# Optimization experiments

Measured on AMD Instinct MI355X. Metric: run time of the kernel, lower is better.

Reference implementation:

```python
import jax, jax.numpy as jnp
import numpy as np
import math

HEAD_DIM = 64           # d_model // n_heads // 2
N_HEADS = 8
LAMBDA_INIT = 0.8 - 0.6 * math.exp(-0.3 * 6)  # depth=6
EPS = 1e-5


def setup_inputs() -> dict:
    key = jax.random.key(0)
    ks = jax.random.split(key, 8)
    B, T, S = 2, 2048, 2048
    return {
        "queries": jax.random.normal(ks[0], (B, 2 * N_HEADS, T, HEAD_DIM), jnp.float32),
        "keys": jax.random.normal(ks[1], (B, 2 * N_HEADS, S, HEAD_DIM), jnp.float32),
        "values": jax.random.normal(ks[2], (B, N_HEADS, S, 2 * HEAD_DIM), jnp.float32),
        "lambda_q1": 0.02 * jax.random.normal(ks[3], (HEAD_DIM,), jnp.float32),
        "lambda_k1": 0.02 * jax.random.normal(ks[4], (HEAD_DIM,), jnp.float32),
        "lambda_q2": 0.02 * jax.random.normal(ks[5], (HEAD_DIM,), jnp.float32),
        "lambda_k2": 0.02 * jax.random.normal(ks[6], (HEAD_DIM,), jnp.float32),
        "subln_weight": jnp.ones((2 * HEAD_DIM,), jnp.float32),
        "tgt_len": 2048,
        "src_len": 2048,
        "attn_mask": jnp.zeros((1,), jnp.bool_),
    }


def reference(queries, keys, values, lambda_q1, lambda_k1, lambda_q2, lambda_k2,
              subln_weight, tgt_len, src_len, attn_mask):
    B = queries.shape[0]
    scaling = HEAD_DIM ** -0.5
    q = queries * scaling
    # [B, 2H, T, S]
    attn_w = jnp.einsum('bhtd,bhsd->bhts', q, keys)
    attn_w = jax.nn.softmax(attn_w.astype(jnp.float32), axis=-1).astype(queries.dtype)
    lam1 = jnp.exp(jnp.sum(lambda_q1 * lambda_k1))
    lam2 = jnp.exp(jnp.sum(lambda_q2 * lambda_k2))
    lam_full = lam1 - lam2 + LAMBDA_INIT
    attn_w = attn_w.reshape(B, N_HEADS, 2, tgt_len, src_len)
    attn_w = attn_w[:, :, 0] - lam_full * attn_w[:, :, 1]   # [B, H, T, S]
    attn = jnp.einsum('bhts,bhse->bhte', attn_w, values)    # [B, H, T, 2*HEAD_DIM]
    # RMSNorm over last dim
    normed = attn * jax.lax.rsqrt(jnp.mean(jnp.square(attn.astype(jnp.float32)), axis=-1, keepdims=True) + EPS).astype(attn.dtype)
    normed = normed * subln_weight
    out = normed * (1.0 - LAMBDA_INIT)
    out = out.transpose(0, 2, 1, 3).reshape(B, tgt_len, N_HEADS * 2 * HEAD_DIM)
    return out
```

## Files before the change

### kernel.cpp

```cpp
#include <hip/hip_runtime.h>
#include <math.h>


#define NT    2048
#define D     64
#define DV    128
#define TQ    64
#define TS    32
#define NROUND (NT / (2 * TS))

#define LAMBDA_INIT 0.70082066706704814f
#define OUT_SCALE   0.29917933293295186f

typedef __attribute__((ext_vector_type(8)))  short    short8;
typedef __attribute__((ext_vector_type(4)))  short    short4v;
typedef __attribute__((ext_vector_type(8)))  _Float16 half8;
typedef __attribute__((ext_vector_type(4)))  float    f32x4;
typedef unsigned short u16;
typedef unsigned int   u32;

#define MFMAH(a, b, c)  __builtin_amdgcn_mfma_f32_16x16x32_f16(a, b, c, 0, 0, 0)
#define MFMA16(a, b, c) __builtin_amdgcn_mfma_f32_16x16x32_bf16(a, b, c, 0, 0, 0)

union Hu { half8 v; _Float16 e[8]; u16 s[8]; short8 sv; };

__device__ __forceinline__ u16 f2h(float x) {
    Hu u; u.e[0] = (_Float16)x; return u.s[0];
}

__global__ __launch_bounds__(256) void prep_k(
    const float* __restrict__ Kg,
    const float* __restrict__ lq1, const float* __restrict__ lk1,
    const float* __restrict__ lq2, const float* __restrict__ lk2,
    u16* __restrict__ Kf, float* __restrict__ lamw)
{
    const int bid = blockIdx.x;
    const int t   = threadIdx.x;
    if (bid == 2048) {
        if (t == 0) {
            float t1 = 0.f, t2 = 0.f;
            for (int i = 0; i < D; ++i) {
                t1 = fmaf(lq1[i], lk1[i], t1);
                t2 = fmaf(lq2[i], lk2[i], t2);
            }
            lamw[0] = __expf(t1) - __expf(t2) + LAMBDA_INIT;
        }
        return;
    }
    const int idx = (bid * 256 + t) * 8;
    const float4 a = *(const float4*)(Kg + idx);
    const float4 b = *(const float4*)(Kg + idx + 4);
    Hu H;
    H.e[0] = (_Float16)a.x; H.e[1] = (_Float16)a.y;
    H.e[2] = (_Float16)a.z; H.e[3] = (_Float16)a.w;
    H.e[4] = (_Float16)b.x; H.e[5] = (_Float16)b.y;
    H.e[6] = (_Float16)b.z; H.e[7] = (_Float16)b.w;
    *(short8*)(Kf + idx) = H.sv;
}

__global__ __launch_bounds__(256) void prep_v(const float* __restrict__ Vg,
                                              u16* __restrict__ Vf)
{
    __shared__ u16 th[64 * 136];
    const int i  = blockIdx.x;
    const int t  = threadIdx.x;
    const int bh = i >> 5;
    const int eb = (i >> 4) & 1;
    const int sb = i & 15;
    const size_t vbase = (size_t)bh * NT * DV + (size_t)sb * 128 * DV + eb * 64;
    {
        const int r0 = t >> 4;
        const int c4 = (t & 15) * 4;
        #pragma unroll
        for (int rr = 0; rr < 8; ++rr) {
            const int row = r0 + rr * 16;
            const float4 x = *(const float4*)(Vg + vbase + (size_t)row * DV + c4);
            th[(c4 + 0) * 136 + row] = f2h(x.x);
            th[(c4 + 1) * 136 + row] = f2h(x.y);
            th[(c4 + 2) * 136 + row] = f2h(x.z);
            th[(c4 + 3) * 136 + row] = f2h(x.w);
        }
    }
    __syncthreads();
    const int e  = t >> 2;
    const int g  = t & 3;
    const size_t orow = ((size_t)bh * DV + eb * 64 + e) * NT + sb * 128;
    #pragma unroll
    for (int c = 0; c < 4; ++c) {
        Hu o;
        #pragma unroll
        for (int j = 0; j < 8; ++j)
            o.s[j] = th[e * 136 + g * 32 + 4 * c + (j & 3) + 16 * (j >> 2)];
        *(short8*)(Vf + orow + g * 32 + c * 8) = o.sv;
    }
}

struct SmemF {
    union {
        short8 c[2048];
        struct {
            float epi[2][32][132];
            float lbuf[2][2][2][32];
        } e;
    };
};

__global__ __launch_bounds__(512, 4) void diffattn_mfma10(
    const float* __restrict__ Qg,
    const u16* __restrict__ Kf, const u16* __restrict__ Vf,
    const float* __restrict__ lamw,
    const float* __restrict__ Wg, float* __restrict__ Outg)
{
    __shared__ SmemF sm;

    const int tid    = threadIdx.x;
    const int wv     = tid >> 6;
    const int lane   = tid & 63;
    const int quad   = lane >> 4;
    const int lc     = lane & 15;
    const int stripe = wv & 1;
    const int hh     = (wv >> 1) & 1;
    const int ks     = wv >> 2;
    const int wig    = wv & 3;
    const int qt     = blockIdx.x;
    const int bh     = blockIdx.y;
    const int b      = bh >> 3, h = bh & 7;

    const int head2b = b * 16 + 2 * h;
    const int bh8    = b * 8 + h;
    const float lam  = lamw[0];

    half8 qf[2][2];
    {
        const size_t qhead = (size_t)(head2b + hh) * NT * D;
        #pragma unroll
        for (int nq = 0; nq < 2; ++nq) {
            const int row = qt * TQ + stripe * 32 + nq * 16 + lc;
            #pragma unroll
            for (int k0 = 0; k0 < 2; ++k0) {
                const int d0 = k0 * 32 + quad * 8;
                const float4 x = *(const float4*)(Qg + qhead + (size_t)row * D + d0);
                const float4 y = *(const float4*)(Qg + qhead + (size_t)row * D + d0 + 4);
                Hu q;
                q.e[0] = (_Float16)(x.x * 0.125f); q.e[1] = (_Float16)(x.y * 0.125f);
                q.e[2] = (_Float16)(x.z * 0.125f); q.e[3] = (_Float16)(x.w * 0.125f);
                q.e[4] = (_Float16)(y.x * 0.125f); q.e[5] = (_Float16)(y.y * 0.125f);
                q.e[6] = (_Float16)(y.z * 0.125f); q.e[7] = (_Float16)(y.w * 0.125f);
                qf[nq][k0] = q.v;
            }
        }
    }

    f32x4 O_[2][8];
    #pragma unroll
    for (int nq = 0; nq < 2; ++nq)
        #pragma unroll
        for (int nt = 0; nt < 8; ++nt) O_[nq][nt] = (f32x4){0.f, 0.f, 0.f, 0.f};
    float lac[2] = {0.f, 0.f};

    u32 gK[2], gV[2];
    int kDst[2], vDst[2];
    #pragma unroll
    for (int j = 0; j < 2; ++j) {
        const int ck  = wig * 128 + lane * 2 + j;
        const int hhs = ck >> 8;
        const int n   = (ck >> 3) & 31;
        const int db  = ck & 7;
        gK[j]   = (u32)(((head2b + hhs) * NT + n) * D + db * 8);
        kDst[j] = ks * 512 + hhs * 256 + n * 8 + (db ^ (n & 7));
        const int cv = wig * 128 + lane * 2 + j;
        const int e  = cv >> 2;
        const int u  = cv & 3;
        gV[j]   = (u32)((bh8 * DV + e) * NT + u * 8);
        vDst[j] = 1024 + ks * 512 + e * 4 + (u ^ ((e >> 1) & 3));
    }

    short8 pk[2], pv[2];
    #pragma unroll
    for (int j = 0; j < 2; ++j) {
        pk[j] = *(const short8*)(Kf + gK[j] + (u32)ks * (TS * D));
        pv[j] = *(const short8*)(Vf + gV[j] + (u32)ks * TS);
    }

    u32 kOff[2][2];
    #pragma unroll
    for (int k0 = 0; k0 < 2; ++k0)
        #pragma unroll
        for (int mt = 0; mt < 2; ++mt)
            kOff[k0][mt] = (u32)((ks * 512 + hh * 256 + (mt * 16 + lc) * 8 +
                                  ((4 * k0 + quad) ^ (lc & 7))) * 8);
    u32 vOff[8];
    {
        const int swzv = quad ^ ((lc >> 1) & 3);
        #pragma unroll
        for (int nt = 0; nt < 8; ++nt)
            vOff[nt] = (u32)((1024 + ks * 512 + (nt * 16 + lc) * 4 + swzv) * 8);
    }

    const u16* ldsu = (const u16*)&sm.c[0];

    for (int r = 0; r < NROUND; ++r) {
        sm.c[kDst[0]] = pk[0];
        sm.c[kDst[1]] = pk[1];
        sm.c[vDst[0]] = pv[0];
        sm.c[vDst[1]] = pv[1];
        __syncthreads();

        if (r < NROUND - 1) {
            const u32 tn = (u32)(2 * r + 2 + ks);
            #pragma unroll
            for (int j = 0; j < 2; ++j) {
                pk[j] = *(const short8*)(Kf + gK[j] + tn * (TS * D));
                pv[j] = *(const short8*)(Vf + gV[j] + tn * TS);
            }
        }

        f32x4 sf[2][2];
        #pragma unroll
        for (int mt = 0; mt < 2; ++mt)
            #pragma unroll
            for (int nq = 0; nq < 2; ++nq) sf[mt][nq] = (f32x4){0.f, 0.f, 0.f, 0.f};
        #pragma unroll
        for (int k0 = 0; k0 < 2; ++k0) {
            #pragma unroll
            for (int mt = 0; mt < 2; ++mt) {
                const half8 kfr = *(const half8*)(ldsu + kOff[k0][mt]);
                #pragma unroll
                for (int nq = 0; nq < 2; ++nq)
                    sf[mt][nq] = MFMAH(kfr, qf[nq][k0], sf[mt][nq]);
            }
        }

        half8 a8[2];
        #pragma unroll
        for (int nq = 0; nq < 2; ++nq) {
            Hu a;
            #pragma unroll
            for (int mt = 0; mt < 2; ++mt)
                #pragma unroll
                for (int i = 0; i < 4; ++i) {
                    const float p = __expf(sf[mt][nq][i]);
                    lac[nq] += p;
                    a.e[mt * 4 + i] = (_Float16)p;
                }
            a8[nq] = a.v;
        }

        #pragma unroll
        for (int nt = 0; nt < 8; ++nt) {
            const half8 vfr = *(const half8*)(ldsu + vOff[nt]);
            #pragma unroll
            for (int nq = 0; nq < 2; ++nq)
                O_[nq][nt] = MFMAH(a8[nq], vfr, O_[nq][nt]);
        }

        __syncthreads();
    }

    {
        float s0 = lac[0], s1 = lac[1];
        s0 += __shfl_xor(s0, 16); s0 += __shfl_xor(s0, 32);
        s1 += __shfl_xor(s1, 16); s1 += __shfl_xor(s1, 32);
        if (quad == 0) {
            sm.e.lbuf[hh][ks][stripe][lc]      = s0;
            sm.e.lbuf[hh][ks][stripe][16 + lc] = s1;
        }
    }
    __syncthreads();
    float coef[2][4];
    #pragma unroll
    for (int nq = 0; nq < 2; ++nq)
        #pragma unroll
        for (int i = 0; i < 4; ++i) {
            const int row = nq * 16 + quad * 4 + i;
            const float lt = sm.e.lbuf[hh][0][stripe][row] +
                             sm.e.lbuf[hh][1][stripe][row];
            coef[nq][i] = (hh == 0) ? (1.f / lt) : (-lam / lt);
        }
    __syncthreads();
    const int pid = hh * 2 + ks;
    #pragma unroll
    for (int p = 0; p < 4; ++p) {
        if (pid == p) {
            #pragma unroll
            for (int nq = 0; nq < 2; ++nq)
                #pragma unroll
                for (int i = 0; i < 4; ++i) {
                    const int row = nq * 16 + quad * 4 + i;
                    #pragma unroll
                    for (int nt = 0; nt < 8; ++nt) {
                        const int col = nt * 16 + lc;
                        const float v = O_[nq][nt][i] * coef[nq][i];
                        if (p == 0) sm.e.epi[stripe][row][col] = v;
                        else        sm.e.epi[stripe][row][col] += v;
                    }
                }
        }
        __syncthreads();
    }
    {
        const int r0 = wv * 8 + (lane >> 3);
        const int st = r0 >> 5, ri = r0 & 31;
        const int e0 = (lane & 7) * 16;
        float x[16];
        float ssq = 0.f;
        #pragma unroll
        for (int m = 0; m < 16; m += 4) {
            const float4 t4 = *(const float4*)&sm.e.epi[st][ri][e0 + m];
            x[m] = t4.x; x[m + 1] = t4.y; x[m + 2] = t4.z; x[m + 3] = t4.w;
            ssq += t4.x * t4.x + t4.y * t4.y + t4.z * t4.z + t4.w * t4.w;
        }
        ssq += __shfl_xor(ssq, 1);
        ssq += __shfl_xor(ssq, 2);
        ssq += __shfl_xor(ssq, 4);
        const float rsq = rsqrtf(ssq * (1.f / 128.f) + 1e-5f) * OUT_SCALE;
        const int rowg = qt * TQ + r0;
        const size_t base =
            ((size_t)b * NT + rowg) * (size_t)(8 * DV) + (size_t)h * DV;
        #pragma unroll
        for (int m = 0; m < 16; m += 4) {
            const float4 w4 = *(const float4*)(Wg + e0 + m);
            float4 o4;
            o4.x = x[m] * rsq * w4.x;
            o4.y = x[m + 1] * rsq * w4.y;
            o4.z = x[m + 2] * rsq * w4.z;
            o4.w = x[m + 3] * rsq * w4.w;
            *(float4*)(Outg + base + e0 + m) = o4;
        }
    }
}

__device__ __forceinline__ unsigned short f2bf(float x) {
    unsigned u = __float_as_uint(x);
    return (unsigned short)((u + 0x7fffu + ((u >> 16) & 1u)) >> 16);
}
__device__ __forceinline__ float bf2f(unsigned short h) {
    return __uint_as_float(((unsigned)h) << 16);
}

struct SmemB {
    union {
        struct {
            short8 kh[2][264];
            short8 kl[2][264];
            short8 vh[516];
            short8 vl[516];
            unsigned short ph[2][2560];
            unsigned short pl[2][2560];
        } L;
        float epi[2][32][132];
    };
};

__global__ __launch_bounds__(256, 2) void diffattn_fb(
    const float* __restrict__ Qg, const float* __restrict__ Kg,
    const float* __restrict__ Vg,
    const float* __restrict__ lq1, const float* __restrict__ lk1,
    const float* __restrict__ lq2, const float* __restrict__ lk2,
    const float* __restrict__ Wg, float* __restrict__ Outg)
{
    __shared__ SmemB sm;
    const int tid = threadIdx.x;
    const int wv = tid >> 6, lane = tid & 63;
    const int quad = lane >> 4, lc = lane & 15;
    const int stripe = wv & 1, hh = wv >> 1;
    const int qt = blockIdx.x, bh = blockIdx.y;
    const int b = bh >> 3, h = bh & 7;
    const size_t koff0 = ((size_t)(b * 16 + 2 * h)) * NT * D;
    const size_t voff  = ((size_t)(b * 8 + h)) * NT * DV;
    float t1 = 0.f, t2 = 0.f;
    for (int i = 0; i < D; ++i) {
        t1 = fmaf(lq1[i], lk1[i], t1);
        t2 = fmaf(lq2[i], lk2[i], t2);
    }
    const float lam = __expf(t1) - __expf(t2) + LAMBDA_INIT;
    short8 qfh[2][2], qfl[2][2];
    {
        const size_t qhead = ((size_t)(b * 16 + 2 * h + hh)) * NT * D;
        #pragma unroll
        for (int mt = 0; mt < 2; ++mt)
            #pragma unroll
            for (int k0 = 0; k0 < 2; ++k0) {
                const int row = qt * TQ + stripe * 32 + mt * 16 + lc;
                const int d0  = k0 * 32 + quad * 8;
                const float4 x = *(const float4*)(Qg + qhead + (size_t)row * D + d0);
                const float4 y = *(const float4*)(Qg + qhead + (size_t)row * D + d0 + 4);
                float f[8] = {x.x, x.y, x.z, x.w, y.x, y.y, y.z, y.w};
                #pragma unroll
                for (int j = 0; j < 8; ++j) {
                    const float v = f[j] * 0.125f;
                    const unsigned short hi = f2bf(v);
                    qfh[mt][k0][j] = (short)hi;
                    qfl[mt][k0][j] = (short)f2bf(v - bf2f(hi));
                }
            }
    }
    f32x4 O_[2][8];
    #pragma unroll
    for (int mt = 0; mt < 2; ++mt)
        #pragma unroll
        for (int nt = 0; nt < 8; ++nt) O_[mt][nt] = (f32x4){0.f, 0.f, 0.f, 0.f};
    float m_[2][4], l_[2][4], a_[2][4];
    #pragma unroll
    for (int mt = 0; mt < 2; ++mt)
        #pragma unroll
        for (int i = 0; i < 4; ++i) { m_[mt][i] = -1e30f; l_[mt][i] = 0.f; }
    const int s_hh = tid >> 7;
    const int s_n  = (tid >> 2) & 31;
    const int s_d0 = (tid & 3) * 16;
    const int s_e0 = tid & 31;
    const int s_s0 = ((tid >> 5) & 7) * 4;
    const int s_sb = s_s0 >> 3;
    const int s_hs = (s_s0 & 4) ? 1 : 0;
    for (int kt = 0; kt < NT / TS; ++kt) {
        const int kb = kt * TS;
        __syncthreads();
        {
            const float* kp = Kg + koff0 + (size_t)s_hh * NT * D +
                              (size_t)(kb + s_n) * D + s_d0;
            const float4 x0 = ((const float4*)kp)[0];
            const float4 x1 = ((const float4*)kp)[1];
            const float4 x2 = ((const float4*)kp)[2];
            const float4 x3 = ((const float4*)kp)[3];
            float f[16] = {x0.x, x0.y, x0.z, x0.w, x1.x, x1.y, x1.z, x1.w,
                           x2.x, x2.y, x2.z, x2.w, x3.x, x3.y, x3.z, x3.w};
            short8 c0h, c0l, c1h, c1l;
            #pragma unroll
            for (int j = 0; j < 8; ++j) {
                unsigned short hi = f2bf(f[j]);
                c0h[j] = (short)hi; c0l[j] = (short)f2bf(f[j] - bf2f(hi));
                hi = f2bf(f[8 + j]);
                c1h[j] = (short)hi; c1l[j] = (short)f2bf(f[8 + j] - bf2f(hi));
            }
            const int db0 = s_d0 >> 3;
            sm.L.kh[s_hh][db0 * 33 + s_n]       = c0h;
            sm.L.kl[s_hh][db0 * 33 + s_n]       = c0l;
            sm.L.kh[s_hh][(db0 + 1) * 33 + s_n] = c1h;
            sm.L.kl[s_hh][(db0 + 1) * 33 + s_n] = c1l;
        }
        {
            #pragma unroll
            for (int j = 0; j < 4; ++j) {
                const int e = s_e0 + 32 * j;
                float f[4];
                #pragma unroll
                for (int i = 0; i < 4; ++i)
                    f[i] = Vg[voff + (size_t)(kb + s_s0 + i) * DV + e];
                short4v hi4, lo4;
                #pragma unroll
                for (int i = 0; i < 4; ++i) {
                    const unsigned short hi = f2bf(f[i]);
                    hi4[i] = (short)hi;
                    lo4[i] = (short)f2bf(f[i] - bf2f(hi));
                }
                ((short4v*)&sm.L.vh[s_sb * 129 + e])[s_hs] = hi4;
                ((short4v*)&sm.L.vl[s_sb * 129 + e])[s_hs] = lo4;
            }
        }
        __syncthreads();
        f32x4 s_f[2][2];
        #pragma unroll
        for (int mt = 0; mt < 2; ++mt)
            #pragma unroll
            for (int nt = 0; nt < 2; ++nt) s_f[mt][nt] = (f32x4){0.f, 0.f, 0.f, 0.f};
        #pragma unroll
        for (int k0 = 0; k0 < 2; ++k0)
            #pragma unroll
            for (int nt = 0; nt < 2; ++nt) {
                const short8 kh = sm.L.kh[hh][(4 * k0 + quad) * 33 + nt * 16 + lc];
                const short8 kl = sm.L.kl[hh][(4 * k0 + quad) * 33 + nt * 16 + lc];
                #pragma unroll
                for (int mt = 0; mt < 2; ++mt) {
                    s_f[mt][nt] = MFMA16(qfh[mt][k0], kh, s_f[mt][nt]);
                    s_f[mt][nt] = MFMA16(qfl[mt][k0], kh, s_f[mt][nt]);
                    s_f[mt][nt] = MFMA16(qfh[mt][k0], kl, s_f[mt][nt]);
                }
            }
        #pragma unroll
        for (int mt = 0; mt < 2; ++mt)
            #pragma unroll
            for (int i = 0; i < 4; ++i) {
                const float v0 = s_f[mt][0][i], v1 = s_f[mt][1][i];
                float mx = fmaxf(v0, v1);
                mx = fmaxf(mx, __shfl_xor(mx, 1));
                mx = fmaxf(mx, __shfl_xor(mx, 2));
                mx = fmaxf(mx, __shfl_xor(mx, 4));
                mx = fmaxf(mx, __shfl_xor(mx, 8));
                const float mn = fmaxf(m_[mt][i], mx);
                const float al = __expf(m_[mt][i] - mn);
                const float p0 = __expf(v0 - mn);
                const float p1 = __expf(v1 - mn);
                float rs = p0 + p1;
                rs += __shfl_xor(rs, 1);
                rs += __shfl_xor(rs, 2);
                rs += __shfl_xor(rs, 4);
                rs += __shfl_xor(rs, 8);
                l_[mt][i] = l_[mt][i] * al + rs;
                m_[mt][i] = mn;
                a_[mt][i] = al;
                const int r = stripe * 32 + mt * 16 + quad * 4 + i;
                const unsigned short h0 = f2bf(p0);
                sm.L.ph[hh][r * 40 + lc]      = h0;
                sm.L.pl[hh][r * 40 + lc]      = f2bf(p0 - bf2f(h0));
                const unsigned short h1 = f2bf(p1);
                sm.L.ph[hh][r * 40 + 16 + lc] = h1;
                sm.L.pl[hh][r * 40 + 16 + lc] = f2bf(p1 - bf2f(h1));
            }
        __syncthreads();
        #pragma unroll
        for (int mt = 0; mt < 2; ++mt)
            #pragma unroll
            for (int nt = 0; nt < 8; ++nt)
                #pragma unroll
                for (int i = 0; i < 4; ++i) O_[mt][nt][i] *= a_[mt][i];
        short8 pah[2], pal[2];
        #pragma unroll
        for (int mt = 0; mt < 2; ++mt) {
            const int r = stripe * 32 + mt * 16 + lc;
            pah[mt] = *(const short8*)&sm.L.ph[hh][r * 40 + quad * 8];
            pal[mt] = *(const short8*)&sm.L.pl[hh][r * 40 + quad * 8];
        }
        #pragma unroll
        for (int nt = 0; nt < 8; ++nt) {
            const short8 vh = sm.L.vh[quad * 129 + nt * 16 + lc];
            const short8 vl = sm.L.vl[quad * 129 + nt * 16 + lc];
            #pragma unroll
            for (int mt = 0; mt < 2; ++mt) {
                O_[mt][nt] = MFMA16(pah[mt], vh, O_[mt][nt]);
                O_[mt][nt] = MFMA16(pal[mt], vh, O_[mt][nt]);
                O_[mt][nt] = MFMA16(pah[mt], vl, O_[mt][nt]);
            }
        }
    }
    __syncthreads();
    if (hh == 1) {
        #pragma unroll
        for (int mt = 0; mt < 2; ++mt)
            #pragma unroll
            for (int i = 0; i < 4; ++i) {
                const float inv = lam / l_[mt][i];
                const int r = mt * 16 + quad * 4 + i;
                #pragma unroll
                for (int nt = 0; nt < 8; ++nt)
                    sm.epi[stripe][r][nt * 16 + lc] = O_[mt][nt][i] * inv;
            }
    }
    __syncthreads();
    if (hh == 0) {
        float wvv[8];
        #pragma unroll
        for (int nt = 0; nt < 8; ++nt) wvv[nt] = Wg[nt * 16 + lc];
        #pragma unroll
        for (int mt = 0; mt < 2; ++mt)
            #pragma unroll
            for (int i = 0; i < 4; ++i) {
                const float inv1 = 1.f / l_[mt][i];
                const int r = mt * 16 + quad * 4 + i;
                float od[8];
                float ss = 0.f;
                #pragma unroll
                for (int nt = 0; nt < 8; ++nt) {
                    od[nt] = O_[mt][nt][i] * inv1 - sm.epi[stripe][r][nt * 16 + lc];
                    ss = fmaf(od[nt], od[nt], ss);
                }
                ss += __shfl_xor(ss, 1);
                ss += __shfl_xor(ss, 2);
                ss += __shfl_xor(ss, 4);
                ss += __shfl_xor(ss, 8);
                const float rsq = rsqrtf(ss * (1.f / 128.f) + 1e-5f) * OUT_SCALE;
                const int rowg = qt * TQ + stripe * 32 + r;
                const size_t base =
                    ((size_t)b * NT + rowg) * (size_t)(8 * DV) + (size_t)h * DV;
                #pragma unroll
                for (int nt = 0; nt < 8; ++nt)
                    Outg[base + nt * 16 + lc] = od[nt] * rsq * wvv[nt];
            }
    }
}

extern "C" void kernel_launch(void* const* d_in, const int* in_sizes, int n_in,
                              void* d_out, int out_size, void* d_ws, size_t ws_size,
                              hipStream_t stream) {
    const float* Q   = (const float*)d_in[0];
    const float* K   = (const float*)d_in[1];
    const float* V   = (const float*)d_in[2];
    const float* lq1 = (const float*)d_in[3];
    const float* lk1 = (const float*)d_in[4];
    const float* lq2 = (const float*)d_in[5];
    const float* lk2 = (const float*)d_in[6];
    const float* W   = (const float*)d_in[7];
    float* Out = (float*)d_out;
    const size_t NEED = 2ull * 4194304ull * sizeof(u16) + 16;
    if (ws_size >= NEED) {
        u16*   Kf   = (u16*)d_ws;
        u16*   Vf   = Kf + 4194304;
        float* lamw = (float*)(Vf + 4194304);
        prep_k<<<2049, 256, 0, stream>>>(K, lq1, lk1, lq2, lk2, Kf, lamw);
        prep_v<<<512, 256, 0, stream>>>(V, Vf);
        diffattn_mfma10<<<dim3(NT / TQ, 16), 512, 0, stream>>>(
            Q, Kf, Vf, lamw, W, Out);
    } else {
        diffattn_fb<<<dim3(NT / TQ, 16), 256, 0, stream>>>(
            Q, K, V, lq1, lk1, lq2, lk2, W, Out);
    }
}
```

Baseline: 176.5 us.

## Double-buffer K/V LDS tiles, use exp2 softmax, and fuse K/V prep kernels

The attention loop now keeps two LDS buffers for the K/V tiles. The next tile is stored into the alternate buffer while the current one is consumed, and the global prefetch runs two rounds ahead, so staging overlaps with the QK MFMAs. The 1/8 scale and log2(e) are folded into the Q scale so softmax can use the native exp2. Probabilities are packed to fp16 with cvt_pkrtz and summed with fdot2 against ones, which means the row sum is now taken from the fp16-rounded values. The separate K and V conversion kernels are merged into one launch, and LDS use per block roughly doubles, which may cap how many blocks fit on a CU.

```diff
diff --git a/kernel.cpp b/kernel.cpp
--- a/kernel.cpp
+++ b/kernel.cpp
@@ -11,10 +11,12 @@
 
 #define LAMBDA_INIT 0.70082066706704814f
 #define OUT_SCALE   0.29917933293295186f
+#define QSCALE      0.18033688011112042f
 
 typedef __attribute__((ext_vector_type(8)))  short    short8;
 typedef __attribute__((ext_vector_type(4)))  short    short4v;
 typedef __attribute__((ext_vector_type(8)))  _Float16 half8;
+typedef __attribute__((ext_vector_type(2)))  __fp16   fp16x2;
 typedef __attribute__((ext_vector_type(4)))  float    f32x4;
 typedef unsigned short u16;
 typedef unsigned int   u32;
@@ -22,20 +24,39 @@
 #define MFMAH(a, b, c)  __builtin_amdgcn_mfma_f32_16x16x32_f16(a, b, c, 0, 0, 0)
 #define MFMA16(a, b, c) __builtin_amdgcn_mfma_f32_16x16x32_bf16(a, b, c, 0, 0, 0)
 
+#if __has_builtin(__builtin_amdgcn_exp2f)
+#define EXP2F(x) __builtin_amdgcn_exp2f(x)
+#else
+#define EXP2F(x) exp2f(x)
+#endif
+
 union Hu { half8 v; _Float16 e[8]; u16 s[8]; short8 sv; };
 
 __device__ __forceinline__ u16 f2h(float x) {
     Hu u; u.e[0] = (_Float16)x; return u.s[0];
 }
 
-__global__ __launch_bounds__(256) void prep_k(
-    const float* __restrict__ Kg,
+__global__ __launch_bounds__(256) void prep_kv(
+    const float* __restrict__ Kg, const float* __restrict__ Vg,
     const float* __restrict__ lq1, const float* __restrict__ lk1,
     const float* __restrict__ lq2, const float* __restrict__ lk2,
-    u16* __restrict__ Kf, float* __restrict__ lamw)
+    u16* __restrict__ Kf, u16* __restrict__ Vf, float* __restrict__ lamw)
 {
+    __shared__ u16 th[64 * 136];
     const int bid = blockIdx.x;
     const int t   = threadIdx.x;
+    if (bid < 2048) {
+        const int idx = (bid * 256 + t) * 8;
+        const float4 a = *(const float4*)(Kg + idx);
+        const float4 b = *(const float4*)(Kg + idx + 4);
+        Hu H;
+        H.e[0] = (_Float16)a.x; H.e[1] = (_Float16)a.y;
+        H.e[2] = (_Float16)a.z; H.e[3] = (_Float16)a.w;
+        H.e[4] = (_Float16)b.x; H.e[5] = (_Float16)b.y;
+        H.e[6] = (_Float16)b.z; H.e[7] = (_Float16)b.w;
+        *(short8*)(Kf + idx) = H.sv;
+        return;
+    }
     if (bid == 2048) {
         if (t == 0) {
             float t1 = 0.f, t2 = 0.f;
@@ -47,23 +68,7 @@
         }
         return;
     }
-    const int idx = (bid * 256 + t) * 8;
-    const float4 a = *(const float4*)(Kg + idx);
-    const float4 b = *(const float4*)(Kg + idx + 4);
-    Hu H;
-    H.e[0] = (_Float16)a.x; H.e[1] = (_Float16)a.y;
-    H.e[2] = (_Float16)a.z; H.e[3] = (_Float16)a.w;
-    H.e[4] = (_Float16)b.x; H.e[5] = (_Float16)b.y;
-    H.e[6] = (_Float16)b.z; H.e[7] = (_Float16)b.w;
-    *(short8*)(Kf + idx) = H.sv;
-}
-
-__global__ __launch_bounds__(256) void prep_v(const float* __restrict__ Vg,
-                                              u16* __restrict__ Vf)
-{
-    __shared__ u16 th[64 * 136];
-    const int i  = blockIdx.x;
-    const int t  = threadIdx.x;
+    const int i  = bid - 2049;
     const int bh = i >> 5;
     const int eb = (i >> 4) & 1;
     const int sb = i & 15;
@@ -97,7 +102,7 @@
 
 struct SmemF {
     union {
-        short8 c[2048];
+        short8 c[4096];
         struct {
             float epi[2][32][132];
             float lbuf[2][2][2][32];
@@ -105,7 +110,7 @@
     };
 };
 
-__global__ __launch_bounds__(512, 4) void diffattn_mfma10(
+__global__ __launch_bounds__(512, 4) void diffattn_mfma11(
     const float* __restrict__ Qg,
     const u16* __restrict__ Kf, const u16* __restrict__ Vf,
     const float* __restrict__ lamw,
@@ -142,10 +147,10 @@
                 const float4 x = *(const float4*)(Qg + qhead + (size_t)row * D + d0);
                 const float4 y = *(const float4*)(Qg + qhead + (size_t)row * D + d0 + 4);
                 Hu q;
-                q.e[0] = (_Float16)(x.x * 0.125f); q.e[1] = (_Float16)(x.y * 0.125f);
-                q.e[2] = (_Float16)(x.z * 0.125f); q.e[3] = (_Float16)(x.w * 0.125f);
-                q.e[4] = (_Float16)(y.x * 0.125f); q.e[5] = (_Float16)(y.y * 0.125f);
-                q.e[6] = (_Float16)(y.z * 0.125f); q.e[7] = (_Float16)(y.w * 0.125f);
+                q.e[0] = (_Float16)(x.x * QSCALE); q.e[1] = (_Float16)(x.y * QSCALE);
+                q.e[2] = (_Float16)(x.z * QSCALE); q.e[3] = (_Float16)(x.w * QSCALE);
+                q.e[4] = (_Float16)(y.x * QSCALE); q.e[5] = (_Float16)(y.y * QSCALE);
+                q.e[6] = (_Float16)(y.z * QSCALE); q.e[7] = (_Float16)(y.w * QSCALE);
                 qf[nq][k0] = q.v;
             }
         }
@@ -175,13 +180,6 @@
         vDst[j] = 1024 + ks * 512 + e * 4 + (u ^ ((e >> 1) & 3));
     }
 
-    short8 pk[2], pv[2];
-    #pragma unroll
-    for (int j = 0; j < 2; ++j) {
-        pk[j] = *(const short8*)(Kf + gK[j] + (u32)ks * (TS * D));
-        pv[j] = *(const short8*)(Vf + gV[j] + (u32)ks * TS);
-    }
-
     u32 kOff[2][2];
     #pragma unroll
     for (int k0 = 0; k0 < 2; ++k0)
@@ -199,15 +197,56 @@
 
     const u16* ldsu = (const u16*)&sm.c[0];
 
+    short8 pk[2], pv[2];
+    #pragma unroll
+    for (int j = 0; j < 2; ++j) {
+        pk[j] = *(const short8*)(Kf + gK[j] + (u32)ks * (TS * D));
+        pv[j] = *(const short8*)(Vf + gV[j] + (u32)ks * TS);
+    }
+    sm.c[kDst[0]] = pk[0];
+    sm.c[kDst[1]] = pk[1];
+    sm.c[vDst[0]] = pv[0];
+    sm.c[vDst[1]] = pv[1];
+    {
+        const u32 tn = (u32)(2 + ks);
+        #pragma unroll
+        for (int j = 0; j < 2; ++j) {
+            pk[j] = *(const short8*)(Kf + gK[j] + tn * (TS * D));
+            pv[j] = *(const short8*)(Vf + gV[j] + tn * TS);
+        }
+    }
+    __syncthreads();
+
+    const fp16x2 ones = {(__fp16)1.f, (__fp16)1.f};
+
     for (int r = 0; r < NROUND; ++r) {
-        sm.c[kDst[0]] = pk[0];
-        sm.c[kDst[1]] = pk[1];
-        sm.c[vDst[0]] = pv[0];
-        sm.c[vDst[1]] = pv[1];
-        __syncthreads();
+        const u32 bo = ((u32)(r & 1)) << 14;
+
+        f32x4 sf[2][2];
+        #pragma unroll
+        for (int mt = 0; mt < 2; ++mt)
+            #pragma unroll
+            for (int nq = 0; nq < 2; ++nq) sf[mt][nq] = (f32x4){0.f, 0.f, 0.f, 0.f};
+        #pragma unroll
+        for (int k0 = 0; k0 < 2; ++k0) {
+            #pragma unroll
+            for (int mt = 0; mt < 2; ++mt) {
+                const half8 kfr = *(const half8*)(ldsu + bo + kOff[k0][mt]);
+                #pragma unroll
+                for (int nq = 0; nq < 2; ++nq)
+                    sf[mt][nq] = MFMAH(kfr, qf[nq][k0], sf[mt][nq]);
+            }
+        }
 
         if (r < NROUND - 1) {
-            const u32 tn = (u32)(2 * r + 2 + ks);
+            const int cd = ((r & 1) ^ 1) << 11;
+            sm.c[cd + kDst[0]] = pk[0];
+            sm.c[cd + kDst[1]] = pk[1];
+            sm.c[cd + vDst[0]] = pv[0];
+            sm.c[cd + vDst[1]] = pv[1];
+        }
+        if (r < NROUND - 2) {
+            const u32 tn = (u32)(2 * (r + 2) + ks);
             #pragma unroll
             for (int j = 0; j < 2; ++j) {
                 pk[j] = *(const short8*)(Kf + gK[j] + tn * (TS * D));
@@ -215,40 +254,28 @@
             }
         }
 
-        f32x4 sf[2][2];
-        #pragma unroll
-        for (int mt = 0; mt < 2; ++mt)
-            #pragma unroll
-            for (int nq = 0; nq < 2; ++nq) sf[mt][nq] = (f32x4){0.f, 0.f, 0.f, 0.f};
-        #pragma unroll
-        for (int k0 = 0; k0 < 2; ++k0) {
-            #pragma unroll
-            for (int mt = 0; mt < 2; ++mt) {
-                const half8 kfr = *(const half8*)(ldsu + kOff[k0][mt]);
-                #pragma unroll
-                for (int nq = 0; nq < 2; ++nq)
-                    sf[mt][nq] = MFMAH(kfr, qf[nq][k0], sf[mt][nq]);
-            }
-        }
-
         half8 a8[2];
         #pragma unroll
         for (int nq = 0; nq < 2; ++nq) {
-            Hu a;
+            union { half8 v; fp16x2 h[4]; } a;
+            float ls = lac[nq];
             #pragma unroll
             for (int mt = 0; mt < 2; ++mt)
                 #pragma unroll
-                for (int i = 0; i < 4; ++i) {
-                    const float p = __expf(sf[mt][nq][i]);
-                    lac[nq] += p;
-                    a.e[mt * 4 + i] = (_Float16)p;
+                for (int ip = 0; ip < 2; ++ip) {
+                    const float p0 = EXP2F(sf[mt][nq][2 * ip]);
+                    const float p1 = EXP2F(sf[mt][nq][2 * ip + 1]);
+                    const fp16x2 h2 = __builtin_amdgcn_cvt_pkrtz(p0, p1);
+                    a.h[mt * 2 + ip] = h2;
+                    ls = __builtin_amdgcn_fdot2(h2, ones, ls, false);
                 }
+            lac[nq] = ls;
             a8[nq] = a.v;
         }
 
         #pragma unroll
         for (int nt = 0; nt < 8; ++nt) {
-            const half8 vfr = *(const half8*)(ldsu + vOff[nt]);
+            const half8 vfr = *(const half8*)(ldsu + bo + vOff[nt]);
             #pragma unroll
             for (int nq = 0; nq < 2; ++nq)
                 O_[nq][nt] = MFMAH(a8[nq], vfr, O_[nq][nt]);
@@ -595,9 +622,8 @@
         u16*   Kf   = (u16*)d_ws;
         u16*   Vf   = Kf + 4194304;
         float* lamw = (float*)(Vf + 4194304);
-        prep_k<<<2049, 256, 0, stream>>>(K, lq1, lk1, lq2, lk2, Kf, lamw);
-        prep_v<<<512, 256, 0, stream>>>(V, Vf);
-        diffattn_mfma10<<<dim3(NT / TQ, 16), 512, 0, stream>>>(
+        prep_kv<<<2561, 256, 0, stream>>>(K, V, lq1, lk1, lq2, lk2, Kf, Vf, lamw);
+        diffattn_mfma11<<<dim3(NT / TQ, 16), 512, 0, stream>>>(
             Q, Kf, Vf, lamw, W, Out);
     } else {
         diffattn_fb<<<dim3(NT / TQ, 16), 256, 0, stream>>>(
```

Result: slower. 185.5 us (+5.1%).
